# Performance work log

Measured on AMD Instinct MI355X. Metric: run time of the kernel, lower is better.

## Reference

```python
import jax, jax.numpy as jnp
import numpy as np

B, L, C = 8, 4096, 512
WS, SHIFT, H = 64, 32, 16
HD = C // H
HID = 4 * C


def _ln(x, w, b):
    m = x.mean(-1, keepdims=True)
    v = ((x - m) ** 2).mean(-1, keepdims=True)
    return (x - m) / jnp.sqrt(v + 1e-5) * w + b


def _attn_mask():
    # 0 / -100 mask for shifted windows, shape (nW, WS, WS)
    img = np.zeros((L,), np.float32)
    cnt = 0
    for s in (slice(0, L - WS), slice(L - WS, L - SHIFT), slice(L - SHIFT, L)):
        img[s] = cnt
        cnt += 1
    mw = img.reshape(L // WS, WS)
    d = mw[:, :, None] - mw[:, None, :]
    return jnp.asarray(np.where(d != 0, -100.0, 0.0).astype(np.float32))


def _cpb_coords():
    # log-spaced continuous relative coords, shape (2*WS-1, 1)
    r = np.arange(-(WS - 1), WS, dtype=np.float32) / (WS - 1) * 8.0
    t = np.sign(r) * np.log2(np.abs(r) + 1.0) / np.log2(8.0)
    return jnp.asarray(t[:, None].astype(np.float32))


def _rel_index():
    c = np.arange(WS)
    return jnp.asarray((c[:, None] - c[None, :] + WS - 1).astype(np.int32))


def setup_inputs():
    key = jax.random.key(0)
    ks = jax.random.split(key, 8)
    n = jax.random.normal
    return {
        "x": n(ks[0], (B, L, C), jnp.float32),
        "qkv_w": n(ks[1], (3 * C, C), jnp.float32) * 0.02,
        "q_bias": jnp.zeros((C,), jnp.float32),
        "v_bias": jnp.zeros((C,), jnp.float32),
        "logit_scale": jnp.log(10.0 * jnp.ones((H, 1, 1), jnp.float32)),
        "cpb_w1": n(ks[2], (512, 1), jnp.float32) * 0.02,
        "cpb_b1": jnp.zeros((512,), jnp.float32),
        "cpb_w2": n(ks[3], (H, 512), jnp.float32) * 0.02,
        "proj_w": n(ks[4], (C, C), jnp.float32) * 0.02,
        "proj_b": jnp.zeros((C,), jnp.float32),
        "norm1_w": jnp.ones((C,), jnp.float32),
        "norm1_b": jnp.zeros((C,), jnp.float32),
        "norm2_w": jnp.ones((C,), jnp.float32),
        "norm2_b": jnp.zeros((C,), jnp.float32),
        "fc1_w": n(ks[5], (HID, C), jnp.float32) * 0.02,
        "fc1_b": jnp.zeros((HID,), jnp.float32),
        "fc2_w": n(ks[6], (C, HID), jnp.float32) * 0.02,
        "fc2_b": jnp.zeros((C,), jnp.float32),
    }


def reference(x, qkv_w, q_bias, v_bias, logit_scale, cpb_w1, cpb_b1, cpb_w2,
              proj_w, proj_b, norm1_w, norm1_b, norm2_w, norm2_b,
              fc1_w, fc1_b, fc2_w, fc2_b):
    nW = L // WS
    shortcut = x
    # cyclic shift + window partition
    xs = jnp.roll(x, -SHIFT, axis=1)
    xw = xs.reshape(B * nW, WS, C)
    # qkv with q/v bias only (k bias is zero)
    qkv_b = jnp.concatenate([q_bias, jnp.zeros_like(v_bias), v_bias])
    qkv = (xw @ qkv_w.T + qkv_b).reshape(B * nW, WS, 3, H, HD)
    qkv = qkv.transpose(2, 0, 3, 1, 4)  # (3, B*nW, H, WS, HD)
    q, k, v = qkv[0], qkv[1], qkv[2]
    # cosine attention with learned, clamped per-head temperature
    qn = q / jnp.maximum(jnp.linalg.norm(q, axis=-1, keepdims=True), 1e-12)
    kn = k / jnp.maximum(jnp.linalg.norm(k, axis=-1, keepdims=True), 1e-12)
    attn = jnp.einsum('whnd,whmd->whnm', qn, kn)
    scale = jnp.exp(jnp.minimum(logit_scale, jnp.log(100.0)))  # (H,1,1)
    attn = attn * scale
    # continuous relative position bias via small MLP
    tbl = jax.nn.relu(_cpb_coords() @ cpb_w1.T + cpb_b1) @ cpb_w2.T  # (2WS-1, H)
    bias = tbl[_rel_index()]  # (WS, WS, H)
    bias = 16.0 * jax.nn.sigmoid(bias.transpose(2, 0, 1))  # (H, WS, WS)
    attn = attn + bias[None]
    # shift mask (0 / -100), per window
    mask = _attn_mask()  # (nW, WS, WS)
    attn = attn.reshape(B, nW, H, WS, WS) + mask[None, :, None]
    attn = jax.nn.softmax(attn.reshape(B * nW, H, WS, WS), axis=-1)
    out = jnp.einsum('whnm,whmd->whnd', attn, v)
    out = out.transpose(0, 2, 1, 3).reshape(B * nW, WS, C)
    out = out @ proj_w.T + proj_b
    # window reverse + reverse shift
    out = jnp.roll(out.reshape(B, L, C), SHIFT, axis=1)
    # Swin v2 post-norm residuals
    x1 = shortcut + _ln(out, norm1_w, norm1_b)
    h = jax.nn.gelu(x1 @ fc1_w.T + fc1_b, approximate=False) @ fc2_w.T + fc2_b
    return x1 + _ln(h, norm2_w, norm2_b)
```

## Files before the change

### kernel.cpp

```cpp
#include <hip/hip_runtime.h>
#include <hip/hip_bf16.h>
#include <math.h>

typedef unsigned short u16;
typedef __bf16 bf16x8 __attribute__((ext_vector_type(8)));
typedef float f32x4 __attribute__((ext_vector_type(4)));
typedef unsigned short u16x8 __attribute__((ext_vector_type(8)));
typedef unsigned short u16x4 __attribute__((ext_vector_type(4)));
typedef unsigned short u16x2 __attribute__((ext_vector_type(2)));

#define DEV static __device__ __forceinline__

DEV float b2f(u16 v) { unsigned u = ((unsigned)v) << 16; return __builtin_bit_cast(float, u); }
DEV u16 f2bf(float f) {
  unsigned u = __builtin_bit_cast(unsigned, f);
  u += 0x7fffu + ((u >> 16) & 1u);
  return (u16)(u >> 16);
}

DEV void async16(const void* g, void* l) {
  __builtin_amdgcn_global_load_lds(
      (const __attribute__((address_space(1))) void*)g,
      (__attribute__((address_space(3))) void*)l, 16, 0, 0);
}

__global__ __launch_bounds__(256) void cvt_all_kernel(
    const float* __restrict__ x,  const float* __restrict__ wq,
    const float* __restrict__ wp, const float* __restrict__ w1,
    const float* __restrict__ w2,
    u16* __restrict__ dx, u16* __restrict__ dq, u16* __restrict__ dp,
    u16* __restrict__ d1, u16* __restrict__ d2)
{
  const int i = blockIdx.x * 256 + threadIdx.x;
  const float* s; u16* d; int off;
  if (i < 4194304)      { s = x;  d = dx; off = i; }
  else if (i < 4390912) { s = wq; d = dq; off = i - 4194304; }
  else if (i < 4456448) { s = wp; d = dp; off = i - 4390912; }
  else if (i < 4718592) { s = w1; d = d1; off = i - 4456448; }
  else if (i < 4980736) { s = w2; d = d2; off = i - 4718592; }
  else return;
  float4 v = ((const float4*)s)[off];
  u16x4 o;
  o[0] = f2bf(v.x); o[1] = f2bf(v.y); o[2] = f2bf(v.z); o[3] = f2bf(v.w);
  ((u16x4*)d)[off] = o;
}

__global__ __launch_bounds__(64) void cpb1_kernel(
    const float* __restrict__ w1, const float* __restrict__ b1,
    const float* __restrict__ w2, float* __restrict__ tbl)
{
  const int r = blockIdx.x, h = blockIdx.y;
  const int lane = threadIdx.x;
  float rv = (float)(r - 63) * (8.0f / 63.0f);
  float sgn = (rv > 0.f) ? 1.f : ((rv < 0.f) ? -1.f : 0.f);
  float t = sgn * log2f(fabsf(rv) + 1.f) * (1.f / 3.f);
  float part = 0.f;
  for (int k = lane; k < 512; k += 64) {
    float hid = fmaxf(t * w1[k] + b1[k], 0.f);
    part += hid * w2[h * 512 + k];
  }
  #pragma unroll
  for (int o = 32; o > 0; o >>= 1) part += __shfl_down(part, o);
  if (lane == 0) tbl[r * 16 + h] = part;
}

__global__ __launch_bounds__(256) void cpb2_kernel(
    const float* __restrict__ tbl, float* __restrict__ btbl)
{
  const int h = blockIdx.x;
  for (int idx = threadIdx.x; idx < 4096; idx += 256) {
    int i = idx >> 6, j = idx & 63;
    float v = tbl[(i - j + 63) * 16 + h];
    btbl[h * 4096 + idx] = 16.f / (1.f + __expf(-v));
  }
}

template <int MODE>
__global__ __launch_bounds__(512, 2) void gemm_bt(
    const u16* __restrict__ A, const u16* __restrict__ W,
    const float* __restrict__ bias1, const float* __restrict__ bias2,
    u16* __restrict__ out, int nby, int N, int K)
{
  extern __shared__ __attribute__((aligned(16))) u16 smem[];
  const int tid = threadIdx.x;
  const int lane = tid & 63;
  const int wv = tid >> 6;
  const int q8 = (int)gridDim.x >> 3;
  const int swb = (blockIdx.x & 7) * q8 + (blockIdx.x >> 3);
  const int m0 = (swb / nby) * 256;
  const int n0 = (swb % nby) * 256;
  const int wm = (wv >> 2) * 128;
  const int wn = (wv & 3) * 64;
  const int fr = lane & 15;
  const int hi = lane >> 4;
  const int srow = tid >> 3;
  const int kb = (tid & 7) ^ (srow & 7);
  f32x4 acc[8][4] = {};

  auto stageA = [&](int buf, int k0, int i) {
    const int r = srow + (i << 6);
    const u16* src;
    if constexpr (MODE == 0) {
      const int mg = m0 + r;
      const int bb = mg >> 12;
      const int p = mg & 4095;
      const long ga = ((long)bb << 12) + ((p + 32) & 4095);
      src = A + ga * (long)K + k0 + kb * 8;
    } else if constexpr (MODE == 1) {
      const int kk = k0 + kb * 8;
      src = A + (size_t)(kk >> 5) * 1048576 + (size_t)(m0 + r) * 32 + (kk & 31);
    } else {
      src = A + (size_t)(m0 + r) * K + k0 + kb * 8;
    }
    async16(src, smem + buf * 16384 + ((i << 9) + tid) * 8);
  };
  auto stageB = [&](int buf, int k0, int i) {
    const int r = srow + (i << 6);
    async16(W + (size_t)(n0 + r) * K + k0 + kb * 8,
            smem + 32768 + buf * 16384 + ((i << 9) + tid) * 8);
  };
  auto stage_part = [&](int buf, int k0, int part) {
    if (part == 0)      { stageB(buf, k0, 0); stageB(buf, k0, 1); }
    else if (part == 1) { stageB(buf, k0, 2); stageB(buf, k0, 3); }
    else if (part == 2) { stageA(buf, k0, 0); stageA(buf, k0, 2); }
    else                { stageA(buf, k0, 1); stageA(buf, k0, 3); }
  };

  auto phase_compute = [&](const u16* lac, const u16* lbc, int mh, int ks) {
    bf16x8 fa[4], fb[4];
    const int sw = hi + (ks << 2);
    #pragma unroll
    for (int mi = 0; mi < 4; ++mi) {
      const int r = wm + ((mh << 2) + mi) * 16 + fr;
      fa[mi] = *(const bf16x8*)&lac[r * 64 + ((sw ^ (r & 7)) << 3)];
    }
    #pragma unroll
    for (int ni = 0; ni < 4; ++ni) {
      const int r = wn + ni * 16 + fr;
      fb[ni] = *(const bf16x8*)&lbc[r * 64 + ((sw ^ (r & 7)) << 3)];
    }
    asm volatile("s_waitcnt lgkmcnt(0)" ::: "memory");
    __builtin_amdgcn_sched_barrier(0);
    __builtin_amdgcn_s_setprio(1);
    #pragma unroll
    for (int mi = 0; mi < 4; ++mi)
      #pragma unroll
      for (int ni = 0; ni < 4; ++ni)
        acc[(mh << 2) + mi][ni] = __builtin_amdgcn_mfma_f32_16x16x32_bf16(
            fa[mi], fb[ni], acc[(mh << 2) + mi][ni], 0, 0, 0);
    __builtin_amdgcn_s_setprio(0);
  };

  const int NT = K >> 6;
  stage_part(0, 0, 0); stage_part(0, 0, 1); stage_part(0, 0, 2); stage_part(0, 0, 3);
  int cur = 0;
  for (int kt = 0; kt < NT; ++kt) {
    const bool hn = (kt + 1) < NT;
    const int nk0 = (kt + 1) << 6;
    const u16* lac = smem + cur * 16384;
    const u16* lbc = smem + 32768 + cur * 16384;
    const int nb = cur ^ 1;
    asm volatile("s_waitcnt vmcnt(2)" ::: "memory");
    __builtin_amdgcn_s_barrier();
    if (hn) stage_part(nb, nk0, 0);
    phase_compute(lac, lbc, 0, 0);
    if (hn) { asm volatile("s_waitcnt vmcnt(2)" ::: "memory"); }
    else    { asm volatile("s_waitcnt vmcnt(0)" ::: "memory"); }
    __builtin_amdgcn_s_barrier();
    if (hn) stage_part(nb, nk0, 1);
    phase_compute(lac, lbc, 1, 0);
    if (hn) stage_part(nb, nk0, 2);
    phase_compute(lac, lbc, 0, 1);
    if (hn) stage_part(nb, nk0, 3);
    phase_compute(lac, lbc, 1, 1);
    cur ^= 1;
  }

  const int lrow = hi * 4;
  #pragma unroll
  for (int mi = 0; mi < 8; ++mi) {
    #pragma unroll
    for (int ni = 0; ni < 4; ++ni) {
      const int n = n0 + wn + ni * 16 + fr;
      #pragma unroll
      for (int r = 0; r < 4; ++r) {
        const int m = m0 + wm + mi * 16 + lrow + r;
        float v = acc[mi][ni][r];
        if constexpr (MODE == 0) {
          const int which = n >> 9, c = n & 511;
          const int hh = c >> 5, d = c & 31;
          float bias = (which == 0) ? bias1[c] : (which == 2 ? bias2[c] : 0.f);
          const int g = m >> 6, ii = m & 63;
          out[(size_t)which * 16777216 + (size_t)g * 32768 + hh * 2048 + ii * 32 + d] =
              f2bf(v + bias);
        } else if constexpr (MODE == 2) {
          float t = v + bias1[n];
          float u = t * t;
          float z = t * (1.5957691216f + 0.0713548163f * u);
          float ge = t / (1.f + __expf(-z));
          out[(size_t)m * N + n] = f2bf(ge);
        } else {
          out[(size_t)m * N + n] = f2bf(v + bias1[n]);
        }
      }
    }
  }
}

__global__ __launch_bounds__(256) void gemm_sm3(
    const u16* __restrict__ A, const u16* __restrict__ W,
    const float* __restrict__ bias1,
    u16* __restrict__ out, int nby, int N, int K)
{
  __shared__ __attribute__((aligned(16))) u16 lA[2][8192];
  __shared__ __attribute__((aligned(16))) u16 lB[2][8192];
  const int tid = threadIdx.x;
  const int wid = tid >> 6;
  const int lane = tid & 63;
  const int q8 = (int)gridDim.x >> 3;
  const int swb = (blockIdx.x & 7) * q8 + (blockIdx.x >> 3);
  const int m0 = (swb / nby) * 128;
  const int n0 = (swb % nby) * 128;
  const int wm = (wid >> 1) * 64;
  const int wn = (wid & 1) * 64;
  f32x4 acc[4][4] = {};

  const int srow8 = lane >> 3;
  const int kel = ((lane & 7) ^ srow8) * 8;

  auto stage = [&](int b, int k0) {
    #pragma unroll
    for (int cc = 0; cc < 4; ++cc) {
      const int rb = wid * 32 + cc * 8;
      const int r = rb + srow8;
      async16(A + (size_t)(m0 + r) * K + k0 + kel, &lA[b][rb * 64]);
      async16(W + (size_t)(n0 + r) * K + k0 + kel, &lB[b][rb * 64]);
    }
  };

  const int NT = K >> 6;
  stage(0, 0);
  __syncthreads();
  int cur = 0;
  const int fr = lane & 15;
  const int hi = lane >> 4;
  const int fsw = fr & 7;
  for (int kt = 0; kt < NT; ++kt) {
    if (kt + 1 < NT) stage(cur ^ 1, (kt + 1) << 6);
    #pragma unroll
    for (int ks = 0; ks < 2; ++ks) {
      bf16x8 fa[4], fb[4];
      #pragma unroll
      for (int t = 0; t < 4; ++t) {
        const int ra = wm + t * 16 + fr;
        fa[t] = *(const bf16x8*)&lA[cur][ra * 64 + (((hi + 4 * ks) ^ fsw) << 3)];
        const int rbq = wn + t * 16 + fr;
        fb[t] = *(const bf16x8*)&lB[cur][rbq * 64 + (((hi + 4 * ks) ^ fsw) << 3)];
      }
      #pragma unroll
      for (int mi = 0; mi < 4; ++mi)
        #pragma unroll
        for (int ni = 0; ni < 4; ++ni)
          acc[mi][ni] = __builtin_amdgcn_mfma_f32_16x16x32_bf16(fa[mi], fb[ni], acc[mi][ni], 0, 0, 0);
    }
    __syncthreads();
    cur ^= 1;
  }

  const int lrow = (lane >> 4) * 4;
  #pragma unroll
  for (int mi = 0; mi < 4; ++mi)
    #pragma unroll
    for (int ni = 0; ni < 4; ++ni) {
      const int n = n0 + wn + ni * 16 + fr;
      #pragma unroll
      for (int r = 0; r < 4; ++r) {
        const int m = m0 + wm + mi * 16 + lrow + r;
        out[(size_t)m * N + n] = f2bf(acc[mi][ni][r] + bias1[n]);
      }
    }
}

__global__ __launch_bounds__(256) void attn_kernel(
    const u16* __restrict__ qkv, const float* __restrict__ ls,
    const float* __restrict__ btbl, u16* __restrict__ attnT)
{
  const int gg = blockIdx.x;
  const int w = threadIdx.x >> 6;
  const int lane = threadIdx.x & 63;
  __shared__ __attribute__((aligned(16))) u16 vt[4][2048];
  __shared__ __attribute__((aligned(16))) u16 pl[4][4096];
  const bool maskw = ((gg & 63) == 63);
  const int fr = lane & 15;
  const int fkq = (lane >> 4) * 8;
  const int crow = (lane >> 4) * 4;

  for (int t = 0; t < 4; ++t) {
    const int h = w * 4 + t;
    const size_t bgh = (size_t)gg * 32768 + (size_t)h * 2048;

    {
      const u16x8* vp = (const u16x8*)(qkv + 33554432 + bgh + (size_t)lane * 32);
      #pragma unroll
      for (int c = 0; c < 4; ++c) {
        u16x8 vr = vp[c];
        #pragma unroll
        for (int e = 0; e < 8; ++e) {
          const int d = c * 8 + e;
          const int addr = d * 64 + (((lane >> 3) ^ (d & 7)) << 3) + (lane & 7);
          vt[w][addr] = vr[e];
        }
      }
    }

    const float scale = __expf(fminf(ls[h], 4.6051701859880914f));
    bf16x8 qa[4], kb[4];
    #pragma unroll
    for (int mi = 0; mi < 4; ++mi) {
      u16x8 raw = *(const u16x8*)(qkv + bgh + (size_t)(mi * 16 + fr) * 32 + fkq);
      float f[8]; float ssum = 0.f;
      #pragma unroll
      for (int e = 0; e < 8; ++e) { f[e] = b2f(raw[e]); ssum += f[e] * f[e]; }
      ssum += __shfl_xor(ssum, 16); ssum += __shfl_xor(ssum, 32);
      const float mul = scale / fmaxf(sqrtf(ssum), 1e-12f);
      u16x8 tmp;
      #pragma unroll
      for (int e = 0; e < 8; ++e) tmp[e] = f2bf(f[e] * mul);
      qa[mi] = __builtin_bit_cast(bf16x8, tmp);
    }
    #pragma unroll
    for (int ni = 0; ni < 4; ++ni) {
      u16x8 raw = *(const u16x8*)(qkv + 16777216 + bgh + (size_t)(ni * 16 + fr) * 32 + fkq);
      float f[8]; float ssum = 0.f;
      #pragma unroll
      for (int e = 0; e < 8; ++e) { f[e] = b2f(raw[e]); ssum += f[e] * f[e]; }
      ssum += __shfl_xor(ssum, 16); ssum += __shfl_xor(ssum, 32);
      const float mul = 1.f / fmaxf(sqrtf(ssum), 1e-12f);
      u16x8 tmp;
      #pragma unroll
      for (int e = 0; e < 8; ++e) tmp[e] = f2bf(f[e] * mul);
      kb[ni] = __builtin_bit_cast(bf16x8, tmp);
    }

    f32x4 s[4][4] = {};
    __builtin_amdgcn_s_setprio(1);
    #pragma unroll
    for (int mi = 0; mi < 4; ++mi)
      #pragma unroll
      for (int ni = 0; ni < 4; ++ni)
        s[mi][ni] = __builtin_amdgcn_mfma_f32_16x16x32_bf16(qa[mi], kb[ni], s[mi][ni], 0, 0, 0);
    __builtin_amdgcn_s_setprio(0);

    const float mh = scale + 16.f;
    float inv_[4][4];
    #pragma unroll
    for (int mi = 0; mi < 4; ++mi) {
      #pragma unroll
      for (int r = 0; r < 4; ++r) {
        const int row = mi * 16 + crow + r;
        float es = 0.f;
        #pragma unroll
        for (int ni = 0; ni < 4; ++ni) {
          const int col = ni * 16 + fr;
          float sv = s[mi][ni][r] + btbl[h * 4096 + row * 64 + col];
          if (maskw && ((row < 32) != (col < 32))) sv -= 100.f;
          const float e = __expf(sv - mh);
          s[mi][ni][r] = e;
          es += e;
        }
        es += __shfl_xor(es, 1); es += __shfl_xor(es, 2);
        es += __shfl_xor(es, 4); es += __shfl_xor(es, 8);
        inv_[mi][r] = 1.f / fmaxf(es, 1e-37f);
      }
    }

    #pragma unroll
    for (int mi = 0; mi < 4; ++mi)
      #pragma unroll
      for (int r = 0; r < 4; ++r) {
        const int row = mi * 16 + crow + r;
        #pragma unroll
        for (int ni = 0; ni < 4; ++ni) {
          const int col = ni * 16 + fr;
          const int addr = row * 64 + (((col >> 3) ^ (row & 7)) << 3) + (col & 7);
          pl[w][addr] = f2bf(s[mi][ni][r]);
        }
      }
    __syncthreads();

    f32x4 o[4][2] = {};
    #pragma unroll
    for (int ks = 0; ks < 2; ++ks) {
      bf16x8 vbf[2];
      #pragma unroll
      for (int np = 0; np < 2; ++np) {
        const int d = np * 16 + fr;
        const int jb = (lane >> 4) + ks * 4;
        vbf[np] = *(const bf16x8*)&vt[w][d * 64 + ((jb ^ (d & 7)) << 3)];
      }
      __builtin_amdgcn_s_setprio(1);
      #pragma unroll
      for (int mp = 0; mp < 4; ++mp) {
        const int row = mp * 16 + fr;
        const int cb = (lane >> 4) + ks * 4;
        bf16x8 paf = *(const bf16x8*)&pl[w][row * 64 + ((cb ^ (row & 7)) << 3)];
        o[mp][0] = __builtin_amdgcn_mfma_f32_16x16x32_bf16(paf, vbf[0], o[mp][0], 0, 0, 0);
        o[mp][1] = __builtin_amdgcn_mfma_f32_16x16x32_bf16(paf, vbf[1], o[mp][1], 0, 0, 0);
      }
      __builtin_amdgcn_s_setprio(0);
    }

    #pragma unroll
    for (int mp = 0; mp < 4; ++mp)
      #pragma unroll
      for (int r = 0; r < 4; ++r) {
        const int row = mp * 16 + crow + r;
        const float iv = inv_[mp][r];
        u16* op = attnT + (size_t)h * 1048576 + (size_t)(gg * 64 + row) * 32;
        op[fr]      = f2bf(o[mp][0][r] * iv);
        op[16 + fr] = f2bf(o[mp][1][r] * iv);
      }
    __syncthreads();
  }
}

__global__ __launch_bounds__(256) void ln1_kernel(
    const u16* __restrict__ proj, const float* __restrict__ x,
    const float* __restrict__ w, const float* __restrict__ bb,
    u16* __restrict__ x1h)
{
  const int t = blockIdx.x;
  const int b = t >> 12, l = t & 4095;
  const int p = (l - 32) & 4095;
  const size_t srow = (((size_t)b << 12) + p) << 9;
  const int c0 = threadIdx.x * 2;
  u16x2 pv = *(const u16x2*)(proj + srow + c0);
  float v0 = b2f(pv[0]), v1 = b2f(pv[1]);
  float s = v0 + v1, ss = v0 * v0 + v1 * v1;
  #pragma unroll
  for (int o = 32; o > 0; o >>= 1) { s += __shfl_down(s, o); ss += __shfl_down(ss, o); }
  __shared__ float red[8];
  const int wid = threadIdx.x >> 6, lane = threadIdx.x & 63;
  if (lane == 0) { red[wid] = s; red[4 + wid] = ss; }
  __syncthreads();
  const float S = red[0] + red[1] + red[2] + red[3];
  const float SS = red[4] + red[5] + red[6] + red[7];
  const float mean = S * (1.f / 512.f);
  const float var = SS * (1.f / 512.f) - mean * mean;
  const float rstd = rsqrtf(var + 1e-5f);
  const size_t orow = (size_t)t << 9;
  float2 xv = *(const float2*)(x + orow + c0);
  const float r0 = xv.x + (v0 - mean) * rstd * w[c0] + bb[c0];
  const float r1 = xv.y + (v1 - mean) * rstd * w[c0 + 1] + bb[c0 + 1];
  u16x2 ho; ho[0] = f2bf(r0); ho[1] = f2bf(r1);
  *(u16x2*)(x1h + orow + c0) = ho;
}

__global__ __launch_bounds__(256) void ln2_kernel(
    const u16* __restrict__ fc2, const u16* __restrict__ x1h,
    const float* __restrict__ w, const float* __restrict__ bb,
    float* __restrict__ out)
{
  const int t = blockIdx.x;
  const size_t row = (size_t)t << 9;
  const int c0 = threadIdx.x * 2;
  u16x2 pv = *(const u16x2*)(fc2 + row + c0);
  float v0 = b2f(pv[0]), v1 = b2f(pv[1]);
  float s = v0 + v1, ss = v0 * v0 + v1 * v1;
  #pragma unroll
  for (int o = 32; o > 0; o >>= 1) { s += __shfl_down(s, o); ss += __shfl_down(ss, o); }
  __shared__ float red[8];
  const int wid = threadIdx.x >> 6, lane = threadIdx.x & 63;
  if (lane == 0) { red[wid] = s; red[4 + wid] = ss; }
  __syncthreads();
  const float S = red[0] + red[1] + red[2] + red[3];
  const float SS = red[4] + red[5] + red[6] + red[7];
  const float mean = S * (1.f / 512.f);
  const float var = SS * (1.f / 512.f) - mean * mean;
  const float rstd = rsqrtf(var + 1e-5f);
  u16x2 xv = *(const u16x2*)(x1h + row + c0);
  const float r0 = b2f(xv[0]) + (v0 - mean) * rstd * w[c0] + bb[c0];
  const float r1 = b2f(xv[1]) + (v1 - mean) * rstd * w[c0 + 1] + bb[c0 + 1];
  float2 fo; fo.x = r0; fo.y = r1;
  *(float2*)(out + row + c0) = fo;
}

extern "C" void kernel_launch(void* const* d_in, const int* in_sizes, int n_in,
                              void* d_out, int out_size, void* d_ws, size_t ws_size,
                              hipStream_t stream) {
  const float* x        = (const float*)d_in[0];
  const float* qkv_w    = (const float*)d_in[1];
  const float* q_bias   = (const float*)d_in[2];
  const float* v_bias   = (const float*)d_in[3];
  const float* lscale   = (const float*)d_in[4];
  const float* cpb_w1   = (const float*)d_in[5];
  const float* cpb_b1   = (const float*)d_in[6];
  const float* cpb_w2   = (const float*)d_in[7];
  const float* proj_w   = (const float*)d_in[8];
  const float* proj_b   = (const float*)d_in[9];
  const float* n1w      = (const float*)d_in[10];
  const float* n1b      = (const float*)d_in[11];
  const float* n2w      = (const float*)d_in[12];
  const float* n2b      = (const float*)d_in[13];
  const float* fc1_w    = (const float*)d_in[14];
  const float* fc1_b    = (const float*)d_in[15];
  const float* fc2_w    = (const float*)d_in[16];
  const float* fc2_b    = (const float*)d_in[17];

  if (ws_size < 134217728u) return;
  char* ws = (char*)d_ws;
  u16* wqkv   = (u16*)(ws + 0);
  u16* wproj  = (u16*)(ws + 1572864);
  u16* wfc1   = (u16*)(ws + 2097152);
  u16* wfc2   = (u16*)(ws + 4194304);
  float* btbl = (float*)(ws + 6291456);
  u16* qkv    = (u16*)(ws + 6553600);
  u16* projo  = (u16*)(ws + 6553600);
  u16* hbuf   = (u16*)(ws + 6553600);
  u16* fc2oh  = (u16*)(ws + 73662464);
  u16* x1h    = (u16*)(ws + 94371840);
  float* tbl  = (float*)(ws + 127926272);
  u16* xbf   = (u16*)d_out;
  u16* attnT = (u16*)d_out;
  float* out = (float*)d_out;

  hipFuncSetAttribute((const void*)gemm_bt<0>, hipFuncAttributeMaxDynamicSharedMemorySize, 131072);
  hipFuncSetAttribute((const void*)gemm_bt<1>, hipFuncAttributeMaxDynamicSharedMemorySize, 131072);
  hipFuncSetAttribute((const void*)gemm_bt<2>, hipFuncAttributeMaxDynamicSharedMemorySize, 131072);

  cvt_all_kernel<<<19456, 256, 0, stream>>>(
      x, qkv_w, proj_w, fc1_w, fc2_w, xbf, wqkv, wproj, wfc1, wfc2);
  cpb1_kernel<<<dim3(127, 16), 64, 0, stream>>>(cpb_w1, cpb_b1, cpb_w2, tbl);
  cpb2_kernel<<<16, 256, 0, stream>>>(tbl, btbl);

  gemm_bt<0><<<768, 512, 131072, stream>>>(
      xbf, wqkv, q_bias, v_bias, qkv, 6, 1536, 512);
  attn_kernel<<<512, 256, 0, stream>>>(qkv, lscale, btbl, attnT);
  gemm_bt<1><<<256, 512, 131072, stream>>>(
      attnT, wproj, proj_b, nullptr, projo, 2, 512, 512);
  ln1_kernel<<<32768, 256, 0, stream>>>(projo, x, n1w, n1b, x1h);
  for (int half = 0; half < 2; ++half) {
    const u16* a2 = x1h + (size_t)half * 8388608;
    gemm_bt<2><<<512, 512, 131072, stream>>>(
        a2, wfc1, fc1_b, nullptr, hbuf, 8, 2048, 512);
    gemm_sm3<<<512, 256, 0, stream>>>(
        hbuf, wfc2, fc2_b, fc2oh, 4, 512, 2048);
    ln2_kernel<<<16384, 256, 0, stream>>>(
        fc2oh, a2, n2w, n2b, out + (size_t)half * 8388608);
  }
}
```

Baseline: 442.2 us.

## Replace QKV GEMM with smaller-tile single-buffered kernel for more blocks

Replaces the 256x256-tile, 512-thread, double-buffered QKV GEMM with a dedicated 128x128-tile, 256-thread kernel that uses 16KB of static LDS and an XOR-swizzled K=32 step. The goal is more blocks and higher occupancy (3072 blocks, up to four per CU), so the 768-block launch is not limited by tail effects and low residency. The new kernel has no prefetch overlap, using a sync-load-compute-sync loop, so load latency may be exposed and each block reuses less data.

```diff
diff --git a/kernel.cpp b/kernel.cpp
--- a/kernel.cpp
+++ b/kernel.cpp
@@ -72,6 +72,77 @@
     int i = idx >> 6, j = idx & 63;
     float v = tbl[(i - j + 63) * 16 + h];
     btbl[h * 4096 + idx] = 16.f / (1.f + __expf(-v));
+  }
+}
+
+__global__ __launch_bounds__(256, 4) void gemm_qkv(
+    const u16* __restrict__ A, const u16* __restrict__ W,
+    const float* __restrict__ bias1, const float* __restrict__ bias2,
+    u16* __restrict__ out, int nby, int N, int K)
+{
+  __shared__ __attribute__((aligned(16))) u16 lA[4096];
+  __shared__ __attribute__((aligned(16))) u16 lB[4096];
+  const int tid = threadIdx.x;
+  const int lane = tid & 63;
+  const int wv = tid >> 6;
+  const int q8 = (int)gridDim.x >> 3;
+  const int swb = (blockIdx.x & 7) * q8 + (blockIdx.x >> 3);
+  const int m0 = (swb / nby) * 128;
+  const int n0 = (swb % nby) * 128;
+  const int wm = (wv >> 1) * 64;
+  const int wn = (wv & 1) * 64;
+  const int fr = lane & 15;
+  const int hi = lane >> 4;
+  const int sr = tid >> 2;
+  const int sp = tid & 3;
+  f32x4 acc[4][4] = {};
+
+  for (int k0 = 0; k0 < K; k0 += 32) {
+    #pragma unroll
+    for (int i = 0; i < 2; ++i) {
+      const int r = i * 64 + sr;
+      const int kk = k0 + ((sp ^ ((r >> 1) & 3)) << 3);
+      const int mg = m0 + r;
+      const int bb = mg >> 12;
+      const int p = mg & 4095;
+      const long ga = ((long)bb << 12) + ((p + 32) & 4095);
+      async16(A + ga * (long)K + kk, lA + r * 32 + sp * 8);
+      async16(W + (size_t)(n0 + r) * K + kk, lB + r * 32 + sp * 8);
+    }
+    __syncthreads();
+    bf16x8 fa[4], fb[4];
+    #pragma unroll
+    for (int t = 0; t < 4; ++t) {
+      const int ra = wm + t * 16 + fr;
+      fa[t] = *(const bf16x8*)&lA[ra * 32 + ((hi ^ ((ra >> 1) & 3)) << 3)];
+      const int rb = wn + t * 16 + fr;
+      fb[t] = *(const bf16x8*)&lB[rb * 32 + ((hi ^ ((rb >> 1) & 3)) << 3)];
+    }
+    #pragma unroll
+    for (int mi = 0; mi < 4; ++mi)
+      #pragma unroll
+      for (int ni = 0; ni < 4; ++ni)
+        acc[mi][ni] = __builtin_amdgcn_mfma_f32_16x16x32_bf16(fa[mi], fb[ni], acc[mi][ni], 0, 0, 0);
+    __syncthreads();
+  }
+
+  const int lrow = hi * 4;
+  #pragma unroll
+  for (int mi = 0; mi < 4; ++mi) {
+    #pragma unroll
+    for (int ni = 0; ni < 4; ++ni) {
+      const int n = n0 + wn + ni * 16 + fr;
+      const int which = n >> 9, c = n & 511;
+      const int hh = c >> 5, d = c & 31;
+      const float bias = (which == 0) ? bias1[c] : (which == 2 ? bias2[c] : 0.f);
+      #pragma unroll
+      for (int r = 0; r < 4; ++r) {
+        const int m = m0 + wm + mi * 16 + lrow + r;
+        const int g = m >> 6, ii = m & 63;
+        out[(size_t)which * 16777216 + (size_t)g * 32768 + hh * 2048 + ii * 32 + d] =
+            f2bf(acc[mi][ni][r] + bias);
+      }
+    }
   }
 }
 
@@ -100,13 +171,7 @@
   auto stageA = [&](int buf, int k0, int i) {
     const int r = srow + (i << 6);
     const u16* src;
-    if constexpr (MODE == 0) {
-      const int mg = m0 + r;
-      const int bb = mg >> 12;
-      const int p = mg & 4095;
-      const long ga = ((long)bb << 12) + ((p + 32) & 4095);
-      src = A + ga * (long)K + k0 + kb * 8;
-    } else if constexpr (MODE == 1) {
+    if constexpr (MODE == 1) {
       const int kk = k0 + kb * 8;
       src = A + (size_t)(kk >> 5) * 1048576 + (size_t)(m0 + r) * 32 + (kk & 31);
     } else {
@@ -186,14 +251,7 @@
       for (int r = 0; r < 4; ++r) {
         const int m = m0 + wm + mi * 16 + lrow + r;
         float v = acc[mi][ni][r];
-        if constexpr (MODE == 0) {
-          const int which = n >> 9, c = n & 511;
-          const int hh = c >> 5, d = c & 31;
-          float bias = (which == 0) ? bias1[c] : (which == 2 ? bias2[c] : 0.f);
-          const int g = m >> 6, ii = m & 63;
-          out[(size_t)which * 16777216 + (size_t)g * 32768 + hh * 2048 + ii * 32 + d] =
-              f2bf(v + bias);
-        } else if constexpr (MODE == 2) {
+        if constexpr (MODE == 2) {
           float t = v + bias1[n];
           float u = t * t;
           float z = t * (1.5957691216f + 0.0713548163f * u);
@@ -524,7 +582,6 @@
   u16* attnT = (u16*)d_out;
   float* out = (float*)d_out;
 
-  hipFuncSetAttribute((const void*)gemm_bt<0>, hipFuncAttributeMaxDynamicSharedMemorySize, 131072);
   hipFuncSetAttribute((const void*)gemm_bt<1>, hipFuncAttributeMaxDynamicSharedMemorySize, 131072);
   hipFuncSetAttribute((const void*)gemm_bt<2>, hipFuncAttributeMaxDynamicSharedMemorySize, 131072);
 
@@ -533,8 +590,8 @@
   cpb1_kernel<<<dim3(127, 16), 64, 0, stream>>>(cpb_w1, cpb_b1, cpb_w2, tbl);
   cpb2_kernel<<<16, 256, 0, stream>>>(tbl, btbl);
 
-  gemm_bt<0><<<768, 512, 131072, stream>>>(
-      xbf, wqkv, q_bias, v_bias, qkv, 6, 1536, 512);
+  gemm_qkv<<<3072, 256, 0, stream>>>(
+      xbf, wqkv, q_bias, v_bias, qkv, 12, 1536, 512);
   attn_kernel<<<512, 256, 0, stream>>>(qkv, lscale, btbl, attnT);
   gemm_bt<1><<<256, 512, 131072, stream>>>(
       attnT, wproj, proj_b, nullptr, projo, 2, 512, 512);
```

New measurement: 417.7 us. 5.5% less time.
